# Optimization experiments

Measured on AMD Instinct MI355X. Metric: run time of the kernel, lower is better.

## Reference

```python
import jax, jax.numpy as jnp
import numpy as np
from jax import lax

# --- Clifford algebra Cl(3,0): sig_g = [1,1,1], n_blades = 8 ---
SIG = np.array([1.0, 1.0, 1.0], dtype=np.float32)
N_GEN = len(SIG)
N_BLADES = 1 << N_GEN

def _build_cayley(g):
    # Structure constants C[a,b,c]: e_a * e_b = C[a,b,a^b] * e_{a^b}
    n = len(g); nb = 1 << n
    C = np.zeros((nb, nb, nb), dtype=np.float32)
    for a in range(nb):
        for b in range(nb):
            s = 1.0
            x = a >> 1
            while x:
                if bin(x & b).count('1') % 2:
                    s = -s
                x >>= 1
            common = a & b
            for k in range(n):
                if (common >> k) & 1:
                    s *= g[k]
            C[a, b, a ^ b] = s
    return C

CAYLEY = _build_cayley(SIG)
# blade signs: scalar coefficient of e_i * e_i (metric square of each blade)
BLADE_SIGNS = np.array([CAYLEY[i, i, 0] for i in range(N_BLADES)], dtype=np.float32)

DT = 0.1      # EPEngine dt
N_FREE = 5    # EPEngine n_free

def _energy(h, input_mv, W_rec, C, signs):
    # h: [B,L,H,I]
    rho = jnp.clip(h, 0.0, 1.0)
    E_self = 0.5 * jnp.sum(h * h, axis=(1, 2, 3))                       # [B]
    E_in = jnp.einsum('blhi,blhi,i->b', rho, input_mv, signs)           # [B]
    # causal recurrent term: geometric product of h_{l-1} with W_rec
    rec = jnp.einsum('blhi,ghj,ijk->blgk', rho[:, :-1], W_rec, C)       # [B,L-1,H,I]
    E_rec = jnp.einsum('blhk,blhk,k->b', rho[:, 1:], rec, signs)        # [B]
    return E_self - E_in - E_rec

def _free_phase(h0, input_mv, W_rec, C, signs):
    gfn = jax.grad(lambda h: jnp.sum(_energy(h, input_mv, W_rec, C, signs)))
    def step(h, _):
        return h - DT * gfn(h), None
    h, _ = lax.scan(step, h0, None, length=N_FREE)
    return h

def setup_inputs() -> dict:
    key = jax.random.key(0)
    ks = jax.random.split(key, 5)
    B, L, V, E, H = 4, 256, 32000, 256, 256
    x = jax.random.randint(ks[0], (B, L), 0, V)
    emb_table = jax.random.normal(ks[1], (V, E), jnp.float32)
    W_in = jax.random.normal(ks[2], (H, E, N_BLADES), jnp.float32) * 0.1
    W_rec = jax.random.normal(ks[3], (H, H, N_BLADES), jnp.float32) * 0.05
    W_out = jax.random.normal(ks[4], (V, H, N_BLADES), jnp.float32) * 0.1
    return {"x": x, "emb_table": emb_table, "W_in": W_in, "W_rec": W_rec, "W_out": W_out}

def reference(x, emb_table, W_in, W_rec, W_out):
    C = jnp.asarray(CAYLEY)
    signs = jnp.asarray(BLADE_SIGNS)
    emb = emb_table[x]                                  # [B,L,E]
    input_mv = jnp.einsum('bld,hdi->blhi', emb, W_in)   # [B,L,H,I]
    B, L = x.shape
    H = W_in.shape[0]
    h0 = jnp.zeros((B, L, H, N_BLADES), jnp.float32)
    h_free = _free_phase(h0, input_mv, W_rec, C, signs) # [B,L,H,I]
    # scalar part of geometric product of h_free with W_out (only blade 0 kept)
    logits = jnp.einsum('blhi,vhj,ij->blv', h_free, W_out, C[:, :, 0])
    return logits
```

## Files before the change

### kernel.cpp

```cpp
#include <hip/hip_runtime.h>
#include <cstddef>
#include <cstdint>

#define VOCAB  32000
#define EMB    256
#define NB     8
#define KDIM   2048
#define NROWS  1024
#define NCOL   4096
#define LLEN   256

typedef __attribute__((ext_vector_type(8))) short short8;
typedef __attribute__((ext_vector_type(4))) float f32x4;
typedef __attribute__((ext_vector_type(16))) float f32x16;
typedef __attribute__((ext_vector_type(4))) int i32x4;
typedef __attribute__((ext_vector_type(16))) int i32x16;

__device__ __forceinline__ float cl3_sign(int a, int b) {
  int x = a >> 1, p = 0;
  while (x) { p ^= __popc(x & b) & 1; x >>= 1; }
  return p ? -1.f : 1.f;
}

__device__ __forceinline__ float clipf(float v) { return fminf(fmaxf(v, 0.f), 1.f); }

__device__ __forceinline__ unsigned short f2bf(float f) {
  unsigned u = __float_as_uint(f);
  u += 0x7FFF + ((u >> 16) & 1);
  return (unsigned short)(u >> 16);
}
__device__ __forceinline__ float bf2f(unsigned short h) {
  return __uint_as_float(((unsigned)h) << 16);
}

__device__ __forceinline__ size_t tso128(int tr, int tk, int r, int kk) {
  return ((size_t)(tr * 64 + tk) << 12) + ((size_t)((kk >> 3) & 3) << 10) + (r << 3) + (kk & 7);
}

__device__ __forceinline__ void gload16(const void* g, void* l) {
  __builtin_amdgcn_global_load_lds((const __attribute__((address_space(1))) uint32_t*)g,
                                   (__attribute__((address_space(3))) uint32_t*)l, 16, 0, 0);
}

__device__ __forceinline__ float dig_inv(float mx) {
  return exp2f((float)(5 - ilogbf(fmaxf(mx, 1e-20f))));
}

__global__ void k_build_mrt_split(const float* __restrict__ Wrec,
                                  unsigned short* __restrict__ Mhi,
                                  unsigned short* __restrict__ Mlo) {
  int idx = blockIdx.x * blockDim.x + threadIdx.x;
  int k = idx & (KDIM - 1);
  int n = idx >> 11;
  int h = k >> 3, i = k & 7;
  float v;
  if (n < KDIM) {
    int g = n >> 3, kb = n & 7;
    int j = i ^ kb;
    v = Wrec[(size_t)g * KDIM + h * NB + j] * cl3_sign(i, j);
  } else {
    int c = n - KDIM;
    int p = c >> 3, q = c & 7;
    int j = q ^ i;
    v = cl3_sign(i, i) * cl3_sign(q, j) * Wrec[(size_t)h * KDIM + p * NB + j];
  }
  unsigned short hi = f2bf(v);
  unsigned short lo = f2bf(v - bf2f(hi));
  size_t off = tso128(n >> 7, k >> 5, n & 127, k & 31);
  Mhi[off] = hi; Mlo[off] = lo;
}

__global__ __launch_bounds__(256) void k_wout_max(const float* __restrict__ W, float* __restrict__ scl) {
  __shared__ float red[256];
  const int t = threadIdx.x;
  size_t stride = (size_t)gridDim.x * 256;
  float m = 0.f;
  for (size_t i = (size_t)blockIdx.x * 256 + t; i < (size_t)VOCAB * KDIM / 4; i += stride) {
    float4 v = ((const float4*)W)[i];
    m = fmaxf(m, fmaxf(fmaxf(fabsf(v.x), fabsf(v.y)), fmaxf(fabsf(v.z), fabsf(v.w))));
  }
  red[t] = m; __syncthreads();
  for (int s = 128; s; s >>= 1) { if (t < s) red[t] = fmaxf(red[t], red[t + s]); __syncthreads(); }
  if (t == 0) atomicMax((unsigned*)(scl + 1), __float_as_uint(red[0]));
}

__global__ __launch_bounds__(256) void k_dig_wout(const float* __restrict__ W,
                                                  const float* __restrict__ scl,
                                                  char* __restrict__ Wd1,
                                                  char* __restrict__ Wd2) {
  __shared__ char l1[16384], l2[16384];
  const int tn = blockIdx.x >> 5;
  const int kt = blockIdx.x & 31;
  const int t = threadIdx.x;
  const float inv = dig_inv(scl[1]);
#pragma unroll
  for (int p = 0; p < 8; ++p) {
    int ci = p * 256 + t;
    int row = ci >> 3, koff = (ci & 7) * 8;
    const float* src = W + (size_t)(tn * 256 + row) * KDIM + kt * 64 + koff;
    float e[8];
    *(float4*)&e[0] = *(const float4*)src;
    *(float4*)&e[4] = *(const float4*)(src + 4);
    char d1[8], d2[8];
#pragma unroll
    for (int j = 0; j < 8; ++j) {
      float tv = e[j] * inv;
      float f1 = rintf(tv);
      d1[j] = (char)(int)f1;
      d2[j] = (char)(int)rintf((tv - f1) * 128.f);
    }
    int lo = ((koff >> 4) << 12) + (row << 4) + (koff & 8);
    *(uint64_t*)&l1[lo] = *(uint64_t*)d1;
    *(uint64_t*)&l2[lo] = *(uint64_t*)d2;
  }
  __syncthreads();
  size_t ob = ((size_t)blockIdx.x << 14) + t * 64;
#pragma unroll
  for (int q = 0; q < 4; ++q) {
    *(i32x4*)&Wd1[ob + q * 16] = *(const i32x4*)&l1[t * 64 + q * 16];
    *(i32x4*)&Wd2[ob + q * 16] = *(const i32x4*)&l2[t * 64 + q * 16];
  }
}

__global__ __launch_bounds__(256) void k_input_mv(const int* __restrict__ x,
                                                  const float* __restrict__ emb,
                                                  const float* __restrict__ Win,
                                                  float* __restrict__ out) {
  __shared__ float se[4][EMB];
  int r0 = blockIdx.x * 4;
  int t = threadIdx.x;
  for (int rr = 0; rr < 4; ++rr) {
    int tok = x[r0 + rr];
    se[rr][t] = emb[(size_t)tok * EMB + t];
  }
  __syncthreads();
  float acc[4][8];
#pragma unroll
  for (int rr = 0; rr < 4; ++rr)
#pragma unroll
    for (int i = 0; i < 8; ++i) acc[rr][i] = 0.f;
  const float* wrow = Win + (size_t)t * KDIM;
  for (int d = 0; d < EMB; ++d) {
    float4 w0 = *(const float4*)(wrow + d * 8);
    float4 w1 = *(const float4*)(wrow + d * 8 + 4);
#pragma unroll
    for (int rr = 0; rr < 4; ++rr) {
      float e = se[rr][d];
      acc[rr][0] += e * w0.x; acc[rr][1] += e * w0.y;
      acc[rr][2] += e * w0.z; acc[rr][3] += e * w0.w;
      acc[rr][4] += e * w1.x; acc[rr][5] += e * w1.y;
      acc[rr][6] += e * w1.z; acc[rr][7] += e * w1.w;
    }
  }
  for (int rr = 0; rr < 4; ++rr) {
    float4* o = (float4*)(out + (size_t)(r0 + rr) * KDIM + t * 8);
    o[0] = make_float4(acc[rr][0], acc[rr][1], acc[rr][2], acc[rr][3]);
    o[1] = make_float4(acc[rr][4], acc[rr][5], acc[rr][6], acc[rr][7]);
  }
}

__global__ __launch_bounds__(256, 2) void k_gemm_pre(const unsigned short* __restrict__ Ahi,
                                                     const unsigned short* __restrict__ Alo,
                                                     const unsigned short* __restrict__ Bhi,
                                                     const unsigned short* __restrict__ Blo,
                                                     float* __restrict__ RF0,
                                                     float* __restrict__ RF1) {
  __shared__ __align__(16) unsigned short lds[2][4][4096];
  const int b = blockIdx.x;
  const int lin = (b & 7) * 64 + (b >> 3);
  const int half = lin >> 8;
  const int inner = lin & 255;
  const int tn = inner >> 3, tm = inner & 7;
  const int ktbase = half << 5;
  float* __restrict__ C = half ? RF1 : RF0;
  const int t = threadIdx.x;
  const int l = t & 63, w = t >> 6;
  const int wr = w >> 1, wc = w & 1;

  const unsigned short* aH = Ahi + ((size_t)tm * 64 << 12);
  const unsigned short* aL = Alo + ((size_t)tm * 64 << 12);
  const unsigned short* bH = Bhi + ((size_t)tn * 64 << 12);
  const unsigned short* bL = Blo + ((size_t)tn * 64 << 12);

  const int ldso0 = w * 1024;
  const int ldso1 = ldso0 + 512;
  const int srco0 = ldso0 + (l << 3);
  const int srco1 = ldso1 + (l << 3);

  const int rA0 = wr * 64 + (l & 31);
  const int rB0 = wc * 64 + (l & 31);
  const int ch0 = l >> 5;

  f32x16 acc[2][2];
#pragma unroll
  for (int i = 0; i < 2; ++i)
#pragma unroll
    for (int j = 0; j < 2; ++j) acc[i][j] = (f32x16)0.f;

  auto STAGE = [&](int bf, int kt) {
    size_t kb = (size_t)kt << 12;
    gload16(aH + kb + srco0, &lds[bf][0][ldso0]);
    gload16(aH + kb + srco1, &lds[bf][0][ldso1]);
    gload16(aL + kb + srco0, &lds[bf][1][ldso0]);
    gload16(aL + kb + srco1, &lds[bf][1][ldso1]);
    gload16(bH + kb + srco0, &lds[bf][2][ldso0]);
    gload16(bH + kb + srco1, &lds[bf][2][ldso1]);
    gload16(bL + kb + srco0, &lds[bf][3][ldso0]);
    gload16(bL + kb + srco1, &lds[bf][3][ldso1]);
  };

  STAGE(0, ktbase);
  __syncthreads();
  int cur = 0;
  for (int it = 0; it < 32; ++it) {
    if (it < 31) STAGE(cur ^ 1, ktbase + it + 1);
#pragma unroll
    for (int s = 0; s < 2; ++s) {
      const int cb = (s * 2 + ch0) << 10;
      short8 ah[2], al[2], bh[2], bl[2];
#pragma unroll
      for (int mi = 0; mi < 2; ++mi) {
        ah[mi] = *(const short8*)&lds[cur][0][cb + ((rA0 + mi * 32) << 3)];
        al[mi] = *(const short8*)&lds[cur][1][cb + ((rA0 + mi * 32) << 3)];
      }
#pragma unroll
      for (int nj = 0; nj < 2; ++nj) {
        bh[nj] = *(const short8*)&lds[cur][2][cb + ((rB0 + nj * 32) << 3)];
        bl[nj] = *(const short8*)&lds[cur][3][cb + ((rB0 + nj * 32) << 3)];
      }
#pragma unroll
      for (int mi = 0; mi < 2; ++mi)
#pragma unroll
        for (int nj = 0; nj < 2; ++nj) {
          acc[mi][nj] = __builtin_amdgcn_mfma_f32_32x32x16_bf16(ah[mi], bh[nj], acc[mi][nj], 0, 0, 0);
          acc[mi][nj] = __builtin_amdgcn_mfma_f32_32x32x16_bf16(ah[mi], bl[nj], acc[mi][nj], 0, 0, 0);
          acc[mi][nj] = __builtin_amdgcn_mfma_f32_32x32x16_bf16(al[mi], bh[nj], acc[mi][nj], 0, 0, 0);
        }
    }
    __syncthreads();
    cur ^= 1;
  }

  const int rg0 = tm * 128 + wr * 64 + ((l >> 5) << 2);
  const int cg0 = tn * 128 + wc * 64 + (l & 31);
#pragma unroll
  for (int mi = 0; mi < 2; ++mi)
#pragma unroll
    for (int nj = 0; nj < 2; ++nj) {
      f32x16 v = acc[mi][nj];
#pragma unroll
      for (int g = 0; g < 16; ++g) {
        int rr = (g & 3) + ((g >> 2) << 3);
        C[(size_t)(rg0 + mi * 32 + rr) * NCOL + cg0 + nj * 32] = v[g];
      }
    }
}

__global__ __launch_bounds__(512, 1) void k_gemm_i8(const char* __restrict__ Ad1,
                                                    const char* __restrict__ Ad2,
                                                    const char* __restrict__ Bd1,
                                                    const char* __restrict__ Bd2,
                                                    const float* __restrict__ scl,
                                                    const float* __restrict__ sA,
                                                    float* __restrict__ C) {
  __shared__ __align__(16) char lds[3 * 49152];
  const int b = blockIdx.x;
  const int lin = (b & 7) * 125 + (b >> 3);
  const int tm = lin & 7, tn = lin >> 3;
  const int t = threadIdx.x;
  const int l = t & 63, w = t >> 6;
  const int wr = w >> 2, wc = w & 3;

  const char* a1g = Ad1 + ((size_t)tm * 32 << 13) + (t << 4);
  const char* a2g = Ad2 + ((size_t)tm * 32 << 13) + (t << 4);
  const char* b1g = Bd1 + ((size_t)tn * 32 << 14) + (t << 4);
  const char* b2g = Bd2 + ((size_t)tn * 32 << 14) + (t << 4);
  const int wub = w << 10;

  const int la = (l & 31) << 4;
  const int rowa0 = (wr * 64 + 0) << 4, rowa1 = (wr * 64 + 32) << 4;
  const int rowb0 = (wc * 64 + 0) << 4, rowb1 = (wc * 64 + 32) << 4;
  const int kqh = (l >> 5) << 1;

  i32x16 acc1[2][2], acc2[2][2];
#pragma unroll
  for (int i = 0; i < 2; ++i)
#pragma unroll
    for (int j = 0; j < 2; ++j) { acc1[i][j] = (i32x16)0; acc2[i][j] = (i32x16)0; }

  auto STAGE_H = [&](int bf, int kt, int h) {
    char* lb = &lds[bf * 49152];
    size_t ka = (size_t)kt << 13, kb = (size_t)kt << 14;
    if (h == 0) {
      gload16(a1g + ka, lb + wub);
      gload16(a2g + ka, lb + 8192 + wub);
      gload16(b1g + kb, lb + 16384 + wub);
    } else {
      gload16(b1g + kb + 8192, lb + 24576 + wub);
      gload16(b2g + kb, lb + 32768 + wub);
      gload16(b2g + kb + 8192, lb + 40960 + wub);
    }
  };

  STAGE_H(0, 0, 0); STAGE_H(0, 0, 1);
  STAGE_H(1, 1, 0); STAGE_H(1, 1, 1);

  int cur = 0;
  for (int kt = 0; kt < 32; ++kt) {
    int pf = cur + 2; if (pf >= 3) pf -= 3;
    if (kt < 31) { asm volatile("s_waitcnt vmcnt(6)" ::: "memory"); }
    else         { asm volatile("s_waitcnt vmcnt(0)" ::: "memory"); }
    __builtin_amdgcn_s_barrier();
    const char* lb = &lds[cur * 49152];
#pragma unroll
    for (int s = 0; s < 2; ++s) {
      const int kqa = ((s << 1) + (l >> 5)) << 11;
      const int kqb = ((s << 1) + (l >> 5)) << 12;
      i32x4 a1[2], a2[2], b1[2], b2[2];
      a1[0] = *(const i32x4*)(lb + kqa + rowa0 + la);
      a1[1] = *(const i32x4*)(lb + kqa + rowa1 + la);
      a2[0] = *(const i32x4*)(lb + 8192 + kqa + rowa0 + la);
      a2[1] = *(const i32x4*)(lb + 8192 + kqa + rowa1 + la);
      b1[0] = *(const i32x4*)(lb + 16384 + kqb + rowb0 + la);
      b1[1] = *(const i32x4*)(lb + 16384 + kqb + rowb1 + la);
      b2[0] = *(const i32x4*)(lb + 32768 + kqb + rowb0 + la);
      b2[1] = *(const i32x4*)(lb + 32768 + kqb + rowb1 + la);
      if (kt + 2 < 32) STAGE_H(pf, kt + 2, s);
      __builtin_amdgcn_s_setprio(1);
#pragma unroll
      for (int mi = 0; mi < 2; ++mi)
#pragma unroll
        for (int nj = 0; nj < 2; ++nj) {
          acc1[mi][nj] = __builtin_amdgcn_mfma_i32_32x32x32_i8(a1[mi], b1[nj], acc1[mi][nj], 0, 0, 0);
          acc2[mi][nj] = __builtin_amdgcn_mfma_i32_32x32x32_i8(a1[mi], b2[nj], acc2[mi][nj], 0, 0, 0);
          acc2[mi][nj] = __builtin_amdgcn_mfma_i32_32x32x32_i8(a2[mi], b1[nj], acc2[mi][nj], 0, 0, 0);
        }
      __builtin_amdgcn_s_setprio(0);
    }
    cur = (cur == 2) ? 0 : cur + 1;
  }

  const float sB = exp2f((float)(ilogbf(scl[1]) + 2));
  const int rbase = tm * 128 + wr * 64 + ((l >> 5) << 2);
  const int cbase = tn * 256 + wc * 64 + (l & 31);
#pragma unroll
  for (int mi = 0; mi < 2; ++mi)
#pragma unroll
    for (int nj = 0; nj < 2; ++nj) {
#pragma unroll
      for (int g = 0; g < 16; ++g) {
        int rr = (g & 3) + ((g >> 2) << 3);
        int row = rbase + mi * 32 + rr;
        float c1 = sA[row] * sB * (1.f / 16384.f);
        C[(size_t)row * VOCAB + cbase + nj * 32] =
            fmaf((float)acc2[mi][nj][g], c1 * (1.f / 128.f), (float)acc1[mi][nj][g] * c1);
      }
    }
}

template <int LAST>
__global__ __launch_bounds__(256) void k_update(float* __restrict__ Hb, const float* __restrict__ Imv,
                                                const float* __restrict__ RF0, const float* __restrict__ RF1,
                                                unsigned short* __restrict__ Hhi,
                                                unsigned short* __restrict__ Hlo,
                                                float* __restrict__ sA,
                                                char* __restrict__ Ad1,
                                                char* __restrict__ Ad2,
                                                int big) {
  __shared__ float red[256];
  int tix = threadIdx.x;
  int idx = blockIdx.x * 256 + tix;
  int r = idx >> 8;
  int c = (idx & 255) << 3;
  int m = r & (LLEN - 1);
  const size_t base = (size_t)r * KDIM + c;
  float h[8], f[8];
  *(float4*)&h[0] = *(const float4*)(Hb + base);
  *(float4*)&h[4] = *(const float4*)(Hb + base + 4);
  float4 i0 = *(const float4*)(Imv + base);
  float4 i1 = *(const float4*)(Imv + base + 4);
  f[0] = i0.x; f[1] = i0.y; f[2] = i0.z; f[3] = i0.w;
  f[4] = i1.x; f[5] = i1.y; f[6] = i1.z; f[7] = i1.w;
#pragma unroll
  for (int j = 0; j < 8; ++j) f[j] *= ((0xE8 >> j) & 1) ? -1.f : 1.f;
  if (m >= 1) {
    const float* rp0 = RF0 + (size_t)(r - 1) * NCOL + c;
    const float* rp1 = RF1 + (size_t)(r - 1) * NCOL + c;
#pragma unroll
    for (int j = 0; j < 8; ++j)
      f[j] += (rp0[j] + rp1[j]) * (((0xE8 >> j) & 1) ? -1.f : 1.f);
  }
  if (m < LLEN - 1) {
    const float* rn0 = RF0 + (size_t)(r + 1) * NCOL + KDIM + c;
    const float* rn1 = RF1 + (size_t)(r + 1) * NCOL + KDIM + c;
#pragma unroll
    for (int j = 0; j < 8; ++j) f[j] += rn0[j] + rn1[j];
  }
  float hn[8], av[8];
#pragma unroll
  for (int j = 0; j < 8; ++j) {
    float hv = h[j];
    float dr = (hv > 0.f && hv < 1.f) ? 1.f : ((hv == 0.f || hv == 1.f) ? 0.5f : 0.f);
    hn[j] = hv - 0.1f * (hv - dr * f[j]);
  }
  *(float4*)(Hb + base) = make_float4(hn[0], hn[1], hn[2], hn[3]);
  *(float4*)(Hb + base + 4) = make_float4(hn[4], hn[5], hn[6], hn[7]);
  if (!LAST) {
    short8 h8, l8;
#pragma unroll
    for (int j = 0; j < 8; ++j) {
      float a = clipf(hn[j]);
      unsigned short hi = f2bf(a);
      h8[j] = (short)hi;
      l8[j] = (short)f2bf(a - bf2f(hi));
    }
    size_t off = tso128(r >> 7, c >> 5, r & 127, c & 31);
    *(short8*)&Hhi[off] = h8;
    *(short8*)&Hlo[off] = l8;
  } else {
    if (!big) return;
#pragma unroll
    for (int j = 0; j < 8; ++j) av[j] = hn[j] * (((0xE8 >> j) & 1) ? -1.f : 1.f);
    float lm = 0.f;
#pragma unroll
    for (int j = 0; j < 8; ++j) lm = fmaxf(lm, fabsf(av[j]));
    red[tix] = lm; __syncthreads();
    for (int s = 128; s; s >>= 1) { if (tix < s) red[tix] = fmaxf(red[tix], red[tix + s]); __syncthreads(); }
    float mx = fmaxf(red[0], 1e-20f);
    float inv = dig_inv(mx);
    if (tix == 0) sA[r] = exp2f((float)(ilogbf(mx) + 2));
    char d1[8], d2[8];
#pragma unroll
    for (int j = 0; j < 8; ++j) {
      float tv = av[j] * inv;
      float f1 = rintf(tv);
      d1[j] = (char)(int)f1;
      d2[j] = (char)(int)rintf((tv - f1) * 128.f);
    }
    size_t addr = (((size_t)(r >> 7) * 32 + (tix >> 3)) << 13) + ((size_t)((tix >> 1) & 3) << 11)
                + ((r & 127) << 4) + ((tix & 1) << 3);
    *(uint64_t*)&Ad1[addr] = *(uint64_t*)d1;
    *(uint64_t*)&Ad2[addr] = *(uint64_t*)d2;
  }
}

template <int AMODE>
__global__ __launch_bounds__(256) void k_gemm_split(const float* __restrict__ A,
                                                    const float* __restrict__ B,
                                                    float* __restrict__ C, int ldc) {
  __shared__ unsigned short Ah[128 * 32], Al[128 * 32];
  __shared__ unsigned short Bh[128 * 32], Bl[128 * 32];
  const int t = threadIdx.x;
  const int row0 = blockIdx.y * 128, col0 = blockIdx.x * 128;
  const int l = t & 63, w = t >> 6;
  const int wr = w >> 1, wc = w & 1;
  const int sr = t >> 3;
  const int cc = (t & 7) << 2;
  const int chunkb = cc >> 3;
  const int halfo = (cc >> 2) & 1;
  f32x4 acc[4][4];
#pragma unroll
  for (int i = 0; i < 4; ++i)
#pragma unroll
    for (int j = 0; j < 4; ++j) acc[i][j] = (f32x4)0.f;
  const float sA0 = 1.f;
  const float sA1 = (cc & 4) ? -1.f : 1.f;
  const float sA2 = sA1;
  const float sA3 = -1.f;
  for (int k0 = 0; k0 < KDIM; k0 += 32) {
    float4 va[4], vb[4];
#pragma unroll
    for (int i = 0; i < 4; ++i) {
      va[i] = *(const float4*)(A + (size_t)(row0 + sr + i * 32) * KDIM + k0 + cc);
      vb[i] = *(const float4*)(B + (size_t)(col0 + sr + i * 32) * KDIM + k0 + cc);
    }
    __syncthreads();
#pragma unroll
    for (int i = 0; i < 4; ++i) {
      int row = sr + i * 32;
      int idx = row * 32 + ((chunkb ^ (row & 3)) << 3) + (halfo << 2);
      float4 a = va[i];
      if (AMODE == 0) {
        a.x = clipf(a.x); a.y = clipf(a.y); a.z = clipf(a.z); a.w = clipf(a.w);
      } else {
        a.x *= sA0; a.y *= sA1; a.z *= sA2; a.w *= sA3;
      }
      ushort4 h4, l4;
      h4.x = f2bf(a.x); l4.x = f2bf(a.x - bf2f(h4.x));
      h4.y = f2bf(a.y); l4.y = f2bf(a.y - bf2f(h4.y));
      h4.z = f2bf(a.z); l4.z = f2bf(a.z - bf2f(h4.z));
      h4.w = f2bf(a.w); l4.w = f2bf(a.w - bf2f(h4.w));
      *(ushort4*)&Ah[idx] = h4;
      *(ushort4*)&Al[idx] = l4;
      float4 bb = vb[i];
      h4.x = f2bf(bb.x); l4.x = f2bf(bb.x - bf2f(h4.x));
      h4.y = f2bf(bb.y); l4.y = f2bf(bb.y - bf2f(h4.y));
      h4.z = f2bf(bb.z); l4.z = f2bf(bb.z - bf2f(h4.z));
      h4.w = f2bf(bb.w); l4.w = f2bf(bb.w - bf2f(h4.w));
      *(ushort4*)&Bh[idx] = h4;
      *(ushort4*)&Bl[idx] = l4;
    }
    __syncthreads();
    short8 ah[4], al[4], bh[4], bl[4];
#pragma unroll
    for (int mi = 0; mi < 4; ++mi) {
      int ar = wr * 64 + mi * 16 + (l & 15);
      int kc = (l >> 4) ^ (ar & 3);
      ah[mi] = *(short8*)&Ah[ar * 32 + kc * 8];
      al[mi] = *(short8*)&Al[ar * 32 + kc * 8];
      int br = wc * 64 + mi * 16 + (l & 15);
      int kb = (l >> 4) ^ (br & 3);
      bh[mi] = *(short8*)&Bh[br * 32 + kb * 8];
      bl[mi] = *(short8*)&Bl[br * 32 + kb * 8];
    }
#pragma unroll
    for (int mi = 0; mi < 4; ++mi)
#pragma unroll
      for (int ni = 0; ni < 4; ++ni) {
        acc[mi][ni] = __builtin_amdgcn_mfma_f32_16x16x32_bf16(ah[mi], bh[ni], acc[mi][ni], 0, 0, 0);
        acc[mi][ni] = __builtin_amdgcn_mfma_f32_16x16x32_bf16(ah[mi], bl[ni], acc[mi][ni], 0, 0, 0);
        acc[mi][ni] = __builtin_amdgcn_mfma_f32_16x16x32_bf16(al[mi], bh[ni], acc[mi][ni], 0, 0, 0);
      }
  }
#pragma unroll
  for (int mi = 0; mi < 4; ++mi)
#pragma unroll
    for (int ni = 0; ni < 4; ++ni) {
      int rg = row0 + wr * 64 + mi * 16 + (l >> 4) * 4;
      int cg = col0 + wc * 64 + ni * 16 + (l & 15);
#pragma unroll
      for (int j = 0; j < 4; ++j)
        C[(size_t)(rg + j) * ldc + cg] = acc[mi][ni][j];
    }
}

extern "C" void kernel_launch(void* const* d_in, const int* in_sizes, int n_in,
                              void* d_out, int out_size, void* d_ws, size_t ws_size,
                              hipStream_t stream) {
  const int*   x    = (const int*)d_in[0];
  const float* emb  = (const float*)d_in[1];
  const float* Win  = (const float*)d_in[2];
  const float* Wrec = (const float*)d_in[3];
  const float* Wout = (const float*)d_in[4];
  float* logits = (float*)d_out;

  char* base = (char*)d_ws;
  const size_t MB = 1ull << 20;
  float* Hbuf = (float*)(base + 0);
  float* Imv  = (float*)(base + 8 * MB);
  float* RF0  = (float*)(base + 16 * MB);
  float* RF1  = (float*)(base + 32 * MB);
  unsigned short* Hhi = (unsigned short*)(base + 48 * MB);
  unsigned short* Hlo = (unsigned short*)(base + 52 * MB);
  unsigned short* Mhi = (unsigned short*)(base + 56 * MB);
  unsigned short* Mlo = (unsigned short*)(base + 72 * MB);
  float* scl = (float*)(base + 88 * MB);
  float* sA  = (float*)(base + 88 * MB + 4096);
  char* Wd1  = base + 88 * MB + 8192;
  char* Wd2  = Wd1 + (size_t)VOCAB * KDIM;
  char* Ad1  = (char*)Mhi;
  char* Ad2  = (char*)Mlo;

  const size_t need = (size_t)(Wd2 - base) + (size_t)VOCAB * KDIM;
  const bool big = ws_size >= need;

  hipMemsetAsync(Hbuf, 0, 8 * MB, stream);
  hipMemsetAsync(Hhi, 0, 8 * MB, stream);
  if (big) hipMemsetAsync(scl, 0, 16, stream);
  k_build_mrt_split<<<32768, 256, 0, stream>>>(Wrec, Mhi, Mlo);
  k_input_mv<<<256, 256, 0, stream>>>(x, emb, Win, Imv);
  if (big) {
    k_wout_max<<<2048, 256, 0, stream>>>(Wout, scl);
    k_dig_wout<<<4000, 256, 0, stream>>>(Wout, scl, Wd1, Wd2);
  }

  for (int it = 0; it < 5; ++it) {
    k_gemm_pre<<<512, 256, 0, stream>>>(Hhi, Hlo, Mhi, Mlo, RF0, RF1);
    if (it < 4) k_update<0><<<1024, 256, 0, stream>>>(Hbuf, Imv, RF0, RF1, Hhi, Hlo, sA, Ad1, Ad2, big);
    else        k_update<1><<<1024, 256, 0, stream>>>(Hbuf, Imv, RF0, RF1, Hhi, Hlo, sA, Ad1, Ad2, big);
  }

  if (big) {
    k_gemm_i8<<<1000, 512, 0, stream>>>(Ad1, Ad2, Wd1, Wd2, scl, sA, logits);
  } else {
    k_gemm_split<1><<<dim3(VOCAB / 128, NROWS / 128), 256, 0, stream>>>(Hbuf, Wout, logits, VOCAB);
  }
}
```

Before: 750.5 us.

## Restructure recurrent GEMM into 128x256 tiles with triple-buffered async pipeline

The split-bf16 recurrent GEMM now launches 256 blocks of 512 threads instead of 512 blocks of 256. Each block computes a 128x256 output tile, which raises B-operand reuse per block. The two-stage LDS buffer with __syncthreads becomes a three-stage ring with prefetch two k-steps ahead, explicit vmcnt waits, split staging interleaved with the MFMA phases, and s_setprio around the MFMA work. The goal is to hide global-load latency and cut barrier stalls. In exchange it uses much more LDS per block (one block per CU), halves the grid, and relies on hand-written waitcnt correctness.

```diff
diff --git a/kernel.cpp b/kernel.cpp
--- a/kernel.cpp
+++ b/kernel.cpp
@@ -159,37 +159,31 @@
   }
 }
 
-__global__ __launch_bounds__(256, 2) void k_gemm_pre(const unsigned short* __restrict__ Ahi,
+__global__ __launch_bounds__(512, 1) void k_gemm_pre(const unsigned short* __restrict__ Ahi,
                                                      const unsigned short* __restrict__ Alo,
                                                      const unsigned short* __restrict__ Bhi,
                                                      const unsigned short* __restrict__ Blo,
                                                      float* __restrict__ RF0,
                                                      float* __restrict__ RF1) {
-  __shared__ __align__(16) unsigned short lds[2][4][4096];
+  __shared__ __align__(16) char lds[3 * 49152];
   const int b = blockIdx.x;
-  const int lin = (b & 7) * 64 + (b >> 3);
-  const int half = lin >> 8;
-  const int inner = lin & 255;
-  const int tn = inner >> 3, tm = inner & 7;
+  const int lin = (b & 7) * 32 + (b >> 3);
+  const int half = lin >> 7;
+  const int inner = lin & 127;
+  const int tm = inner & 7, tn = inner >> 3;
   const int ktbase = half << 5;
   float* __restrict__ C = half ? RF1 : RF0;
   const int t = threadIdx.x;
   const int l = t & 63, w = t >> 6;
-  const int wr = w >> 1, wc = w & 1;
-
-  const unsigned short* aH = Ahi + ((size_t)tm * 64 << 12);
-  const unsigned short* aL = Alo + ((size_t)tm * 64 << 12);
-  const unsigned short* bH = Bhi + ((size_t)tn * 64 << 12);
-  const unsigned short* bL = Blo + ((size_t)tn * 64 << 12);
-
-  const int ldso0 = w * 1024;
-  const int ldso1 = ldso0 + 512;
-  const int srco0 = ldso0 + (l << 3);
-  const int srco1 = ldso1 + (l << 3);
-
-  const int rA0 = wr * 64 + (l & 31);
-  const int rB0 = wc * 64 + (l & 31);
-  const int ch0 = l >> 5;
+  const int wr = w >> 2, wc = w & 3;
+
+  const char* aHg  = (const char*)Ahi + (((size_t)tm * 64) << 13) + (t << 4);
+  const char* aLg  = (const char*)Alo + (((size_t)tm * 64) << 13) + (t << 4);
+  const char* bHg0 = (const char*)Bhi + (((size_t)(tn * 2) * 64) << 13) + (t << 4);
+  const char* bHg1 = (const char*)Bhi + (((size_t)(tn * 2 + 1) * 64) << 13) + (t << 4);
+  const char* bLg0 = (const char*)Blo + (((size_t)(tn * 2) * 64) << 13) + (t << 4);
+  const char* bLg1 = (const char*)Blo + (((size_t)(tn * 2 + 1) * 64) << 13) + (t << 4);
+  const int wub = w << 10;
 
   f32x16 acc[2][2];
 #pragma unroll
@@ -197,37 +191,51 @@
 #pragma unroll
     for (int j = 0; j < 2; ++j) acc[i][j] = (f32x16)0.f;
 
-  auto STAGE = [&](int bf, int kt) {
-    size_t kb = (size_t)kt << 12;
-    gload16(aH + kb + srco0, &lds[bf][0][ldso0]);
-    gload16(aH + kb + srco1, &lds[bf][0][ldso1]);
-    gload16(aL + kb + srco0, &lds[bf][1][ldso0]);
-    gload16(aL + kb + srco1, &lds[bf][1][ldso1]);
-    gload16(bH + kb + srco0, &lds[bf][2][ldso0]);
-    gload16(bH + kb + srco1, &lds[bf][2][ldso1]);
-    gload16(bL + kb + srco0, &lds[bf][3][ldso0]);
-    gload16(bL + kb + srco1, &lds[bf][3][ldso1]);
+  auto STAGE_H = [&](int bf, int kt, int hh) {
+    char* lb = &lds[bf * 49152];
+    size_t kb = (size_t)kt << 13;
+    if (hh == 0) {
+      gload16(aHg + kb, lb + wub);
+      gload16(aLg + kb, lb + 8192 + wub);
+      gload16(bHg0 + kb, lb + 16384 + wub);
+    } else {
+      gload16(bHg1 + kb, lb + 24576 + wub);
+      gload16(bLg0 + kb, lb + 32768 + wub);
+      gload16(bLg1 + kb, lb + 40960 + wub);
+    }
   };
 
-  STAGE(0, ktbase);
-  __syncthreads();
+  STAGE_H(0, ktbase, 0); STAGE_H(0, ktbase, 1);
+  STAGE_H(1, ktbase + 1, 0); STAGE_H(1, ktbase + 1, 1);
+
+  const int ra  = wr * 64 + (l & 31);
+  const int rbb = wc * 64 + (l & 31);
   int cur = 0;
-  for (int it = 0; it < 32; ++it) {
-    if (it < 31) STAGE(cur ^ 1, ktbase + it + 1);
+  for (int kt = 0; kt < 32; ++kt) {
+    int pf = cur + 2; if (pf >= 3) pf -= 3;
+    if (kt < 31) { asm volatile("s_waitcnt vmcnt(6)" ::: "memory"); }
+    else         { asm volatile("s_waitcnt vmcnt(0)" ::: "memory"); }
+    __builtin_amdgcn_s_barrier();
+    const char* lb = &lds[cur * 49152];
 #pragma unroll
     for (int s = 0; s < 2; ++s) {
-      const int cb = (s * 2 + ch0) << 10;
+      const int kc = ((s << 1) + (l >> 5)) << 11;
       short8 ah[2], al[2], bh[2], bl[2];
 #pragma unroll
       for (int mi = 0; mi < 2; ++mi) {
-        ah[mi] = *(const short8*)&lds[cur][0][cb + ((rA0 + mi * 32) << 3)];
-        al[mi] = *(const short8*)&lds[cur][1][cb + ((rA0 + mi * 32) << 3)];
+        int off = kc + ((ra + mi * 32) << 4);
+        ah[mi] = *(const short8*)(lb + off);
+        al[mi] = *(const short8*)(lb + 8192 + off);
       }
 #pragma unroll
       for (int nj = 0; nj < 2; ++nj) {
-        bh[nj] = *(const short8*)&lds[cur][2][cb + ((rB0 + nj * 32) << 3)];
-        bl[nj] = *(const short8*)&lds[cur][3][cb + ((rB0 + nj * 32) << 3)];
+        int rb = rbb + nj * 32;
+        int off = ((rb >> 7) << 13) + kc + ((rb & 127) << 4);
+        bh[nj] = *(const short8*)(lb + 16384 + off);
+        bl[nj] = *(const short8*)(lb + 32768 + off);
       }
+      if (kt + 2 < 32) STAGE_H(pf, ktbase + kt + 2, s);
+      __builtin_amdgcn_s_setprio(1);
 #pragma unroll
       for (int mi = 0; mi < 2; ++mi)
 #pragma unroll
@@ -236,13 +244,13 @@
           acc[mi][nj] = __builtin_amdgcn_mfma_f32_32x32x16_bf16(ah[mi], bl[nj], acc[mi][nj], 0, 0, 0);
           acc[mi][nj] = __builtin_amdgcn_mfma_f32_32x32x16_bf16(al[mi], bh[nj], acc[mi][nj], 0, 0, 0);
         }
-    }
-    __syncthreads();
-    cur ^= 1;
+      __builtin_amdgcn_s_setprio(0);
+    }
+    cur = (cur == 2) ? 0 : cur + 1;
   }
 
   const int rg0 = tm * 128 + wr * 64 + ((l >> 5) << 2);
-  const int cg0 = tn * 128 + wc * 64 + (l & 31);
+  const int cg0 = tn * 256 + wc * 64 + (l & 31);
 #pragma unroll
   for (int mi = 0; mi < 2; ++mi)
 #pragma unroll
@@ -280,7 +288,6 @@
   const int la = (l & 31) << 4;
   const int rowa0 = (wr * 64 + 0) << 4, rowa1 = (wr * 64 + 32) << 4;
   const int rowb0 = (wc * 64 + 0) << 4, rowb1 = (wc * 64 + 32) << 4;
-  const int kqh = (l >> 5) << 1;
 
   i32x16 acc1[2][2], acc2[2][2];
 #pragma unroll
@@ -575,7 +582,7 @@
   }
 
   for (int it = 0; it < 5; ++it) {
-    k_gemm_pre<<<512, 256, 0, stream>>>(Hhi, Hlo, Mhi, Mlo, RF0, RF1);
+    k_gemm_pre<<<256, 512, 0, stream>>>(Hhi, Hlo, Mhi, Mlo, RF0, RF1);
     if (it < 4) k_update<0><<<1024, 256, 0, stream>>>(Hbuf, Imv, RF0, RF1, Hhi, Hlo, sA, Ad1, Ad2, big);
     else        k_update<1><<<1024, 256, 0, stream>>>(Hbuf, Imv, RF0, RF1, Hhi, Hlo, sA, Ad1, Ad2, big);
   }
```

New measurement: 743.6 us. Within noise of the previous version (-0.9%).
